# Kernel optimization log

Measured on AMD Instinct MI355X. Metric: run time of the kernel, lower is better.

The kernel has to match this reference:

```python
import jax, jax.numpy as jnp
import numpy as np


def conv2d(x, w, b):
    # x: [D, Cin, H, W], w: [Cout, Cin, kh, kw], SAME padding, stride 1
    y = jax.lax.conv_general_dilated(
        x, w, window_strides=(1, 1), padding='SAME',
        dimension_numbers=('NCHW', 'OIHW', 'NCHW'))
    return y + b[None, :, None, None]


def setup_inputs() -> dict:
    key = jax.random.key(0)
    ks = jax.random.split(key, 12)
    B, N, T, H, W = 2, 3, 16, 28, 28
    Cp, Ch, Ck, Cv, Cs = 1024, 512, 64, 512, 256
    s = 0.02
    return {
        'f16': jax.random.normal(ks[0], (B, Cp, H, W), jnp.float32),
        'mk':  jax.random.normal(ks[1], (B, Ck, T, H, W), jnp.float32),
        'mv':  jax.random.normal(ks[2], (B, N, Cv, T, H, W), jnp.float32),
        'h':   jax.random.normal(ks[3], (B, N, Cs, H, W), jnp.float32),
        # KeyProj: 1x1 conv then 3x3 conv
        'w1': jax.random.normal(ks[4], (Ch, Cp, 1, 1), jnp.float32) * s,
        'b1': jnp.zeros((Ch,), jnp.float32),
        'w2': jax.random.normal(ks[5], (Ck, Ch, 3, 3), jnp.float32) * s,
        'b2': jnp.zeros((Ck,), jnp.float32),
        # sensory-updater transform: 3x3 conv, (Cv+Cs) -> 3*Cs
        'wt': jax.random.normal(ks[6], (3 * Cs, Cv + Cs, 3, 3), jnp.float32) * s,
        'bt': jnp.zeros((3 * Cs,), jnp.float32),
    }


def reference(f16, mk, mv, h, w1, b1, w2, b2, wt, bt):
    B, Ck, T = mk.shape[0], mk.shape[1], mk.shape[2]
    N, Cv = mv.shape[1], mv.shape[2]
    Cs = h.shape[2]
    H, W = f16.shape[-2:]
    P = H * W          # query pixels
    M = T * H * W      # memory slots

    # KeyProj: query key from pixel feature
    qk = conv2d(conv2d(f16, w1, b1), w2, b2)          # [B, Ck, H, W]

    # KV-memory affinity read (softmax over memory axis)
    mk_flat = mk.reshape(B, Ck, M)
    qk_flat = qk.reshape(B, Ck, P)
    logits = jnp.einsum('bcm,bcp->bmp', mk_flat, qk_flat) / jnp.sqrt(
        jnp.asarray(Ck, qk.dtype))                     # [B, M, P]
    aff = jax.nn.softmax(logits, axis=1)               # normalize over memory
    readout = jnp.einsum('bncm,bmp->bncp', mv.reshape(B, N, Cv, M), aff)
    readout = readout.reshape(B, N, Cv, H, W)          # [B, N, Cv, H, W]

    # gated recurrent sensory update (recurrent_update)
    x = jnp.concatenate([readout, h], axis=2).reshape(B * N, Cv + Cs, H, W)
    vals = conv2d(x, wt, bt).reshape(B, N, 3 * Cs, H, W)
    forget_g = jax.nn.sigmoid(vals[:, :, :Cs])
    update_g = jax.nn.sigmoid(vals[:, :, Cs:2 * Cs])
    new_vals = jnp.tanh(vals[:, :, 2 * Cs:])
    new_h = forget_g * h * (1.0 - update_g) + update_g * new_vals
    return new_h
```

## Files before the change

kernel.cpp:

```cpp
#include <hip/hip_runtime.h>

typedef unsigned short u16;
typedef unsigned int u32;
typedef float f32x4v __attribute__((ext_vector_type(4)));
typedef __bf16 bf16x8 __attribute__((ext_vector_type(8)));

#define GAS __attribute__((address_space(1)))
#define LAS __attribute__((address_space(3)))

__device__ __forceinline__ u16 f2bf(float f) {
  u32 u = __builtin_bit_cast(u32, f);
  u32 r = (u + 0x7FFFu + ((u >> 16) & 1u)) >> 16;
  return (u16)r;
}
__device__ __forceinline__ float bf2f(u16 h) {
  return __builtin_bit_cast(float, (u32)h << 16);
}
__device__ __forceinline__ void gld_lds16(const void* g, void* l) {
  __builtin_amdgcn_global_load_lds((const GAS void*)g, (LAS void*)l, 16, 0, 0);
}
#define VMCNT(N) asm volatile("s_waitcnt vmcnt(" #N ")" ::: "memory")
#define MFMA16(a, b, c) __builtin_amdgcn_mfma_f32_16x16x32_bf16((a), (b), (c), 0, 0, 0)

template <int CONV>
__device__ __forceinline__ void gemm8p_dev(
    int lb, int Gpad, const u16* A, const u16* B, u16* Cp,
    int M, int N, int Kc, int fullK, int S,
    long strA, long strB, long strC, int Cin, int gx, int gy, int nwg, u16* smem)
{
  const int cpx = Gpad >> 3;
  const int L = (lb & 7) * cpx + (lb >> 3);
  if (L >= nwg) return;
  const int by = L % gy;
  const int rest = L / gy;
  const int bx = rest % gx;
  const int z = rest / gx;

  const int t = threadIdx.x, lane = t & 63, wave = t >> 6;
  const int zb = z / S, s = z - zb * S;
  const int m0 = bx * 256, n0 = by * 256;
  const int kbeg = s * Kc;
  const int kavail = fullK - kbeg;
  const int kc = Kc < kavail ? Kc : kavail;
  const int T = kc >> 6;

  const int srow = t >> 3;
  const int g = ((t & 7) - (srow & 7)) & 7;
  const int ldsoff = t * 8;

  const u16* Asrc[2][2];
  #pragma unroll
  for (int h = 0; h < 2; ++h)
    #pragma unroll
    for (int q = 0; q < 2; ++q) {
      int r = m0 + h * 128 + q * 64 + srow; if (r >= M) r = M - 1;
      Asrc[h][q] = A + (long)zb * strA + (long)r * fullK + kbeg + g * 8;
    }
  const u16* Bsrc[2][2];
  #pragma unroll
  for (int h = 0; h < 2; ++h)
    #pragma unroll
    for (int q = 0; q < 2; ++q) {
      if constexpr (CONV) {
        int pn = n0 + h * 128 + q * 64 + srow; if (pn >= N) pn = 0;
        const int img = pn / 784, p = pn - img * 784;
        const int py = p / 28, px = p - py * 28;
        Bsrc[h][q] = B + ((long)img * 900 + (py + 1) * 30 + (px + 1)) * Cin + g * 8;
      } else {
        int r = n0 + h * 128 + q * 64 + srow; if (r >= N) r = N - 1;
        Bsrc[h][q] = B + (long)zb * strB + (long)r * fullK + kbeg + g * 8;
      }
    }

  auto stageA = [&](int tile, int h) {
    u16* d = smem + (((tile & 1) * 2 + h) * 8192);
    const long ko = (long)tile * 64;
    gld_lds16(Asrc[h][0] + ko, d + ldsoff);
    gld_lds16(Asrc[h][1] + ko, d + 4096 + ldsoff);
  };
  auto stageB = [&](int tile, int h) {
    u16* d = smem + 32768 + (((tile & 1) * 2 + h) * 8192);
    long off;
    if constexpr (CONV) {
      const int kg = kbeg + tile * 64;
      const int tap = kg / Cin, kc2 = kg - tap * Cin;
      off = (long)((tap / 3 - 1) * 30 + (tap % 3 - 1)) * Cin + kc2;
    } else {
      off = (long)tile * 64;
    }
    gld_lds16(Bsrc[h][0] + off, d + ldsoff);
    gld_lds16(Bsrc[h][1] + off, d + 4096 + ldsoff);
  };

  const int wm = wave & 1, wn = wave >> 1;
  const int lr = lane & 15, hi = lane >> 4;
  const int slot0 = ((hi + (lr & 7)) & 7) * 8;
  const int slot1 = (((hi + 4) + (lr & 7)) & 7) * 8;
  f32x4v acc[8][4] = {};
  bf16x8 breg[4][2];

  stageB(0, 0); stageB(0, 1);
  stageA(0, 0); stageA(0, 1);
  stageB(1, 0); stageB(1, 1);
  VMCNT(4);
  __builtin_amdgcn_s_barrier();

  for (int tau = 0; tau < T; ++tau) {
    const int d = tau & 1;
    const u16* aB = smem + ((d * 2 + wm) * 8192);
    const u16* bB = smem + 32768 + ((d * 2 + (wn >> 1)) * 8192);
    const int ta = (tau + 1 < T) ? tau + 1 : T - 1;
    const int tb = (tau + 2 < T) ? tau + 2 : T - 1;
    #pragma unroll
    for (int Q = 0; Q < 4; ++Q) {
      bf16x8 aph[2][2];
      #pragma unroll
      for (int m2 = 0; m2 < 2; ++m2) {
        const int lrow = (Q * 2 + m2) * 16 + lr;
        aph[m2][0] = *(const bf16x8*)&aB[lrow * 64 + slot0];
        aph[m2][1] = *(const bf16x8*)&aB[lrow * 64 + slot1];
      }
      if (Q == 0) {
        #pragma unroll
        for (int n = 0; n < 4; ++n) {
          const int lrow = (wn & 1) * 64 + n * 16 + lr;
          breg[n][0] = *(const bf16x8*)&bB[lrow * 64 + slot0];
          breg[n][1] = *(const bf16x8*)&bB[lrow * 64 + slot1];
        }
      }
      if      (Q == 0) stageA(ta, 0);
      else if (Q == 1) stageA(ta, 1);
      else if (Q == 2) stageB(tb, 0);
      else             { stageB(tb, 1); VMCNT(4); }
      __builtin_amdgcn_sched_barrier(0);
      __builtin_amdgcn_s_barrier();
      __builtin_amdgcn_s_setprio(1);
      #pragma unroll
      for (int m2 = 0; m2 < 2; ++m2)
        #pragma unroll
        for (int n = 0; n < 4; ++n) {
          acc[Q * 2 + m2][n] = MFMA16(aph[m2][0], breg[n][0], acc[Q * 2 + m2][n]);
          acc[Q * 2 + m2][n] = MFMA16(aph[m2][1], breg[n][1], acc[Q * 2 + m2][n]);
        }
      __builtin_amdgcn_s_setprio(0);
      __builtin_amdgcn_sched_barrier(0);
      __builtin_amdgcn_s_barrier();
    }
  }
  VMCNT(0);

  u16* Co = Cp + (long)z * strC;
  #pragma unroll
  for (int m = 0; m < 8; ++m)
    #pragma unroll
    for (int r = 0; r < 4; ++r) {
      const int row = m0 + wm * 128 + m * 16 + hi * 4 + r;
      if (row >= M) continue;
      #pragma unroll
      for (int n = 0; n < 4; ++n) {
        const int col = n0 + wn * 64 + n * 16 + lr;
        if (col < N) Co[(long)row * N + col] = f2bf(acc[m][n][r]);
      }
    }
}

__device__ __forceinline__ void gemmRC_dev(
    int lb, int Gpad, const u16* A, const u16* B, u16* Cp,
    int M, int N, int Kc, int fullK, int S,
    long strA, long strB, long strC, int gx, int gy, int nwg, u16* smem)
{
  const int cpx = Gpad >> 3;
  const int L = (lb & 7) * cpx + (lb >> 3);
  if (L >= nwg) return;
  const int by = L % gy;
  const int rest = L / gy;
  const int bx = rest % gx;
  const int z = rest / gx;

  u16* sA = smem;
  u16* sB = smem + 3 * 8192;
  const int t = threadIdx.x, lane = t & 63, wave = t >> 6;
  const int zb = z / S, s = z - zb * S;
  const int m0 = bx * 256, n0 = by * 128;
  const int kbeg = s * Kc;
  const int niter = Kc >> 5;

  const int schunk = ((t & 3) ^ ((t >> 4) & 3)) * 8;
  const u16* Ap[2]; const u16* Bp;
  #pragma unroll
  for (int q = 0; q < 2; ++q) {
    int ra = m0 + q * 128 + (t >> 2); if (ra >= M) ra = M - 1;
    Ap[q] = A + (long)zb * strA + (long)ra * fullK + schunk;
  }
  {
    int rb = n0 + (t >> 2); if (rb >= N) rb = N - 1;
    Bp = B + (long)zb * strB + (long)rb * fullK + schunk;
  }
  const int ldst = t * 8;

  auto stage = [&](int buf, int kg) {
    u16* dA = sA + buf * 8192;
    gld_lds16(Ap[0] + kg, &dA[ldst]);
    gld_lds16(Ap[1] + kg, &dA[4096 + ldst]);
    gld_lds16(Bp + kg,    &sB[buf * 4096 + ldst]);
  };

  const int wrow = (wave & 3) * 64, wcol = (wave >> 2) * 64;
  const int lr = lane & 15, hi = lane >> 4;
  const int csw = (hi ^ (lr >> 2)) * 8;
  f32x4v acc[4][4] = {};

  for (int p = 0; p < 2 && p < niter; ++p) stage(p, kbeg + p * 32);
  int cur = 0, nxt = 2;
  for (int it = 0; it < niter; ++it) {
    if (it + 2 < niter) {
      stage(nxt, kbeg + (it + 2) * 32);
      VMCNT(6);
    } else {
      const int rem = niter - 1 - it;
      if (rem == 1) VMCNT(3); else VMCNT(0);
    }
    __builtin_amdgcn_s_barrier();
    __builtin_amdgcn_sched_barrier(0);
    const u16* cA = sA + cur * 8192;
    const u16* cB = sB + cur * 4096;
    bf16x8 af[4], bf[4];
    #pragma unroll
    for (int m = 0; m < 4; ++m) af[m] = *(const bf16x8*)&cA[(wrow + m*16 + lr) * 32 + csw];
    #pragma unroll
    for (int n = 0; n < 4; ++n) bf[n] = *(const bf16x8*)&cB[(wcol + n*16 + lr) * 32 + csw];
    __builtin_amdgcn_s_setprio(1);
    #pragma unroll
    for (int m = 0; m < 4; ++m)
      #pragma unroll
      for (int n = 0; n < 4; ++n)
        acc[m][n] = MFMA16(af[m], bf[n], acc[m][n]);
    __builtin_amdgcn_s_setprio(0);
    __builtin_amdgcn_sched_barrier(0);
    __builtin_amdgcn_s_barrier();
    cur = (cur + 1 == 3) ? 0 : cur + 1;
    nxt = (nxt + 1 == 3) ? 0 : nxt + 1;
  }

  u16* Co = Cp + (long)z * strC;
  const int lq = hi * 4;
  #pragma unroll
  for (int m = 0; m < 4; ++m)
    #pragma unroll
    for (int r = 0; r < 4; ++r) {
      const int row = m0 + wrow + m * 16 + lq + r;
      if (row >= M) continue;
      #pragma unroll
      for (int n = 0; n < 4; ++n) {
        const int col = n0 + wcol + n * 16 + lr;
        if (col < N) Co[(long)row * N + col] = f2bf(acc[m][n][r]);
      }
    }
}

__device__ __forceinline__ void border_slot(int slot, int& py, int& px) {
  if (slot < 30)      { py = 0;         px = slot; }
  else if (slot < 60) { py = 29;        px = slot - 30; }
  else if (slot < 88) { py = slot - 59; px = 0; }
  else                { py = slot - 87; px = 29; }
}

__device__ __forceinline__ void transp_dev(
    const float* in, u16* out, int R, int C, int ldOut,
    int bx, int by, int t, float (*tile)[33])
{
  const int c0 = bx * 32, r0 = by * 32;
  const int tx = t & 31, ty = t >> 5;
  for (int i = ty; i < 32; i += 8) {
    const int r = r0 + i, c = c0 + tx;
    tile[i][tx] = (r < R && c < C) ? in[(long)r * C + c] : 0.0f;
  }
  __syncthreads();
  for (int i = ty; i < 32; i += 8) {
    const int r = r0 + tx, c = c0 + i;
    if (c < C && r < R)
      out[(long)c * ldOut + r] = f2bf(tile[tx][i]);
  }
}

__global__ __launch_bounds__(256) void prep1(
    const float* __restrict__ f16, const float* __restrict__ mk,
    const float* __restrict__ w1, const float* __restrict__ w2,
    const float* __restrict__ wt,
    u16* __restrict__ f16T, u16* __restrict__ mkT, u16* __restrict__ w1b,
    u16* __restrict__ w2R, u16* __restrict__ wtR)
{
  __shared__ float tile[32][33];
  const int bid = blockIdx.x, t = threadIdx.x;
  if (bid < 1600) {
    const int bx = bid % 25, by = (bid / 25) % 32, bz = bid / 800;
    transp_dev(f16 + (long)bz * 1024 * 784, f16T + (long)bz * 784 * 1024,
               1024, 784, 1024, bx, by, t, tile);
    return;
  }
  if (bid < 3168) {
    const int lb = bid - 1600;
    const int bx = lb % 392, by = (lb / 392) % 2, bz = lb / 784;
    transp_dev(mk + (long)bz * 64 * 12544, mkT + (long)bz * 12544 * 64,
               64, 12544, 64, bx, by, t, tile);
    return;
  }
  if (bid < 3424) {
    const long i = (long)(bid - 3168) * 256 + t;
    const float4* p = (const float4*)w1 + i * 2;
    const float4 a = p[0], b = p[1];
    u16 o[8] = {f2bf(a.x), f2bf(a.y), f2bf(a.z), f2bf(a.w),
                f2bf(b.x), f2bf(b.y), f2bf(b.z), f2bf(b.w)};
    ((uint4*)w1b)[i] = *(uint4*)o;
    return;
  }
  if (bid < 4576) {
    const int idx = (bid - 3424) * 256 + t;
    const int c = idx % 512, tap = (idx / 512) % 9, m = idx / 4608;
    w2R[idx] = f2bf(w2[((long)m * 512 + c) * 9 + tap]);
    return;
  }
  const long idx = (long)(bid - 4576) * 256 + t;
  const int c = (int)(idx % 768), tap = (int)((idx / 768) % 9), m = (int)(idx / 6912);
  wtR[idx] = f2bf(wt[((long)m * 768 + c) * 9 + tap]);
}

__global__ __launch_bounds__(512, 4) void fused1(
    const u16* __restrict__ f16T, const u16* __restrict__ w1b,
    u16* __restrict__ parts, u16* __restrict__ out1P)
{
  extern __shared__ u16 smem[];
  const int bid = blockIdx.x, t = threadIdx.x;
  if (bid < 224) {
    gemmRC_dev(bid, 224, f16T, w1b, parts, 1568, 512, 128, 1024, 8,
               0, 0, 1568L * 512, 7, 4, 224, smem);
    return;
  }
  const int gid = (bid - 224) * 512 + t;
  if (gid < 14848) {
    const int c8 = gid & 63, rest = gid >> 6;
    const int slot = rest % 116, img = rest / 116;
    int py, px; border_slot(slot, py, px);
    *(uint4*)&out1P[((long)img * 900 + py * 30 + px) * 512 + c8 * 8] =
        make_uint4(0, 0, 0, 0);
  }
}

__global__ __launch_bounds__(256) void conv2_mv(
    const u16* __restrict__ Wt, const u16* __restrict__ imgP,
    float* __restrict__ Cp, const float* __restrict__ mv, u16* __restrict__ mvb)
{
  __shared__ u16 sA[2][128 * 32];
  __shared__ u16 sB[2][128 * 32];
  const int bid = blockIdx.x, t = threadIdx.x;
  if (bid >= 234) {
    for (long g = (long)(bid - 234) * 256 + t; g < 4816896L; g += 2048L * 256) {
      const float4* p = (const float4*)mv + g * 2;
      const float4 a = p[0], b = p[1];
      u16 o[8] = {f2bf(a.x), f2bf(a.y), f2bf(a.z), f2bf(a.w),
                  f2bf(b.x), f2bf(b.y), f2bf(b.z), f2bf(b.w)};
      ((uint4*)mvb)[g] = *(uint4*)o;
    }
    return;
  }
  const int lane = t & 63, wave = t >> 6;
  const int z = bid / 13;
  const int m0 = 0, n0 = (bid % 13) * 128;
  const int Cin = 512, Ntot = 1568, M = 64, Kc = 256;
  const int kbeg = z * Kc;

  const u16* Aptr[2]; const u16* Bptr[2]; int lofs[2];
  #pragma unroll
  for (int i = 0; i < 2; ++i) {
    const int tp = i * 256 + t;
    const int r = tp >> 2;
    const int c16 = (tp & 3) ^ ((tp >> 4) & 3);
    int ra = m0 + r; if (ra >= M) ra = M - 1;
    int pn = n0 + r; if (pn >= Ntot) pn = 0;
    const int img = pn / 784, p = pn - img * 784;
    const int py = p / 28, px = p - py * 28;
    Aptr[i] = Wt + (long)ra * (9 * Cin) + c16 * 8;
    Bptr[i] = imgP + ((long)img * 900 + (py + 1) * 30 + (px + 1)) * Cin + c16 * 8;
    lofs[i] = (i * 256 + (wave << 6)) * 8;
  }
  auto stage = [&](int buf, int kg) {
    const int tap = kg / Cin, kc = kg - tap * Cin;
    const long off = (long)((tap / 3 - 1) * 30 + (tap % 3 - 1)) * Cin + kc;
    #pragma unroll
    for (int i = 0; i < 2; ++i) {
      gld_lds16(Aptr[i] + kg, &sA[buf][lofs[i]]);
      gld_lds16(Bptr[i] + off, &sB[buf][lofs[i]]);
    }
  };

  const int wr = (wave >> 1) * 64, wc = (wave & 1) * 64;
  const int lr = lane & 15, hi = lane >> 4;
  const int csw = (hi ^ (lr >> 2)) * 8;
  f32x4v acc[4][4] = {};
  const int niter = Kc >> 5;

  stage(0, kbeg);
  for (int it = 0; it < niter; ++it) {
    const int cur = it & 1;
    if (it + 1 < niter) {
      stage(cur ^ 1, kbeg + (it + 1) * 32);
      VMCNT(4);
    } else {
      VMCNT(0);
    }
    __builtin_amdgcn_s_barrier();
    __builtin_amdgcn_sched_barrier(0);
    bf16x8 af[4], bv[4];
    #pragma unroll
    for (int i = 0; i < 4; ++i) af[i] = *(const bf16x8*)&sA[cur][(wr + i*16 + lr) * 32 + csw];
    #pragma unroll
    for (int j = 0; j < 4; ++j) bv[j] = *(const bf16x8*)&sB[cur][(wc + j*16 + lr) * 32 + csw];
    __builtin_amdgcn_s_setprio(1);
    #pragma unroll
    for (int i = 0; i < 4; ++i)
      #pragma unroll
      for (int j = 0; j < 4; ++j)
        acc[i][j] = MFMA16(af[i], bv[j], acc[i][j]);
    __builtin_amdgcn_s_setprio(0);
    __builtin_amdgcn_sched_barrier(0);
    __builtin_amdgcn_s_barrier();
  }

  float* Co = Cp + (long)z * M * Ntot;
  const int lq = hi * 4;
  #pragma unroll
  for (int i = 0; i < 4; ++i)
    #pragma unroll
    for (int r = 0; r < 4; ++r) {
      const int row = m0 + wr + i*16 + lq + r;
      if (row >= M) continue;
      #pragma unroll
      for (int j = 0; j < 4; ++j) {
        const int col = n0 + wc + j*16 + lr;
        if (col < Ntot) Co[(long)row * Ntot + col] = acc[i][j][r];
      }
    }
}

template <int BK>
__global__ __launch_bounds__(256) void gemm_glds(
    const u16* __restrict__ A, const u16* __restrict__ B, u16* __restrict__ C,
    int M, int N, int Kc, int fullK, int S,
    long strA, long strB, long strC, float scale)
{
  constexpr int CPR = BK / 8;
  constexpr int ISS = BK / 16;
  __shared__ u16 sA[2][128 * BK];
  __shared__ u16 sB[2][128 * BK];
  const int t = threadIdx.x, lane = t & 63, wave = t >> 6;
  const int z = blockIdx.z, zb = z / S;
  const int m0 = blockIdx.x * 128, n0 = blockIdx.y * 128;
  const int kbeg = (z - zb * S) * Kc;

  const u16* Aptr[ISS]; const u16* Bptr[ISS]; int lofs[ISS];
  #pragma unroll
  for (int i = 0; i < ISS; ++i) {
    const int tp = i * 256 + t;
    const int r = tp / CPR;
    int c16 = tp % CPR;
    if constexpr (BK == 32) c16 = c16 ^ ((tp >> 4) & 3);
    else                    c16 = (c16 - (r & 7)) & 7;
    int ra = m0 + r; if (ra >= M) ra = M - 1;
    int rb = n0 + r; if (rb >= N) rb = N - 1;
    Aptr[i] = A + (long)zb * strA + (long)ra * fullK + kbeg + c16 * 8;
    Bptr[i] = B + (long)zb * strB + (long)rb * fullK + kbeg + c16 * 8;
    lofs[i] = (i * 256 + (wave << 6)) * 8;
  }
  auto stage = [&](int buf, int k0) {
    #pragma unroll
    for (int i = 0; i < ISS; ++i) {
      gld_lds16(Aptr[i] + k0, &sA[buf][lofs[i]]);
      gld_lds16(Bptr[i] + k0, &sB[buf][lofs[i]]);
    }
  };

  const int wr = (wave >> 1) * 64, wc = (wave & 1) * 64;
  const int lr = lane & 15, hi = lane >> 4;
  f32x4v acc[4][4] = {};
  const int niter = Kc / BK;

  stage(0, 0);
  for (int it = 0; it < niter; ++it) {
    const int cur = it & 1;
    if (it + 1 < niter) {
      stage(cur ^ 1, (it + 1) * BK);
      if constexpr (ISS == 2) VMCNT(4); else VMCNT(8);
    } else {
      VMCNT(0);
    }
    __builtin_amdgcn_s_barrier();
    __builtin_amdgcn_sched_barrier(0);
    #pragma unroll
    for (int kk = 0; kk < BK; kk += 32) {
      bf16x8 af[4], bv[4];
      #pragma unroll
      for (int i = 0; i < 4; ++i) {
        const int row = wr + i*16 + lr;
        int lk;
        if constexpr (BK == 32) lk = kk + ((hi ^ (lr >> 2)) * 8);
        else                    lk = ((((kk >> 3) + hi) + (row & 7)) & 7) * 8;
        af[i] = *(const bf16x8*)&sA[cur][row * BK + lk];
      }
      #pragma unroll
      for (int j = 0; j < 4; ++j) {
        const int row = wc + j*16 + lr;
        int lk;
        if constexpr (BK == 32) lk = kk + ((hi ^ (lr >> 2)) * 8);
        else                    lk = ((((kk >> 3) + hi) + (row & 7)) & 7) * 8;
        bv[j] = *(const bf16x8*)&sB[cur][row * BK + lk];
      }
      __builtin_amdgcn_s_setprio(1);
      #pragma unroll
      for (int i = 0; i < 4; ++i)
        #pragma unroll
        for (int j = 0; j < 4; ++j)
          acc[i][j] = MFMA16(af[i], bv[j], acc[i][j]);
      __builtin_amdgcn_s_setprio(0);
    }
    __builtin_amdgcn_sched_barrier(0);
    __builtin_amdgcn_s_barrier();
  }

  const int lq = hi * 4;
  u16* Cw = C + (long)zb * strC;
  #pragma unroll
  for (int i = 0; i < 4; ++i)
    #pragma unroll
    for (int r = 0; r < 4; ++r) {
      const int row = m0 + wr + i*16 + lq + r;
      if (row >= M) continue;
      #pragma unroll
      for (int j = 0; j < 4; ++j) {
        const int col = n0 + wc + j*16 + lr;
        if (col < N) Cw[(long)row * N + col] = f2bf(acc[i][j][r] * scale);
      }
    }
}

__device__ __forceinline__ void addbf4(float* a, uint2 v) {
  a[0] += bf2f((u16)(v.x & 0xFFFFu));
  a[1] += bf2f((u16)(v.x >> 16));
  a[2] += bf2f((u16)(v.y & 0xFFFFu));
  a[3] += bf2f((u16)(v.y >> 16));
}

__global__ __launch_bounds__(256) void reduce_c1_bf(
    const u16* __restrict__ parts, u16* __restrict__ dst,
    const float* __restrict__ bias, int S)
{
  const long idx = (long)blockIdx.x * 256 + threadIdx.x;
  if (idx >= 1568L * 128) return;
  const int c4 = (int)(idx & 127), p = (int)(idx >> 7);
  const int c = c4 * 4;
  float sum[4] = {bias[c], bias[c+1], bias[c+2], bias[c+3]};
  for (int s = 0; s < S; ++s)
    addbf4(sum, *(const uint2*)&parts[((long)s * 1568 + p) * 512 + c]);
  const int im = p / 784, q = p - im * 784;
  const int qpad = (q / 28 + 1) * 30 + (q % 28 + 1);
  u16 o[4] = {f2bf(sum[0]), f2bf(sum[1]), f2bf(sum[2]), f2bf(sum[3])};
  *(uint2*)&dst[((long)im * 900 + qpad) * 512 + c] = *(uint2*)o;
}

__global__ __launch_bounds__(256) void reduceT_ro(
    const u16* __restrict__ parts, u16* __restrict__ dst, int S)
{
  __shared__ float tile[32][33];
  const int b = blockIdx.z, c0 = blockIdx.x * 32, p0 = blockIdx.y * 32;
  const int tx = threadIdx.x & 31, ty = threadIdx.x >> 5;
  for (int i = ty; i < 32; i += 8) {
    const int pc = min(p0 + tx, 783);
    float s = 0;
    for (int k = 0; k < S; ++k)
      s += bf2f(parts[((long)(b * S + k) * 1536 + c0 + i) * 784 + pc]);
    tile[i][tx] = s;
  }
  __syncthreads();
  for (int i = ty; i < 32; i += 8) {
    const int p = p0 + i, c = c0 + tx;
    if (p < 784) {
      const int n = c >> 9, cc = c & 511;
      const int qpad = (p / 28 + 1) * 30 + (p % 28 + 1);
      dst[((long)(b * 3 + n) * 900 + qpad) * 768 + cc] = f2bf(tile[tx][i]);
    }
  }
}

__global__ __launch_bounds__(256) void reduceT_qk(
    const float* __restrict__ parts, u16* __restrict__ dst,
    const float* __restrict__ bias, int S)
{
  __shared__ float tile[32][33];
  const int b = blockIdx.z, c0 = blockIdx.x * 32, p0 = blockIdx.y * 32;
  const int tx = threadIdx.x & 31, ty = threadIdx.x >> 5;
  for (int i = ty; i < 32; i += 8) {
    const int pc = min(p0 + tx, 783);
    const long base = (long)(c0 + i) * 1568 + b * 784 + pc;
    float s = 0;
    for (int k = 0; k < S; ++k) s += parts[(long)k * 64 * 1568 + base];
    tile[i][tx] = s;
  }
  __syncthreads();
  for (int i = ty; i < 32; i += 8) {
    const int p = p0 + i, c = c0 + tx;
    if (p < 784)
      dst[((long)b * 784 + p) * 64 + c] = f2bf(tile[tx][i] + bias[c]);
  }
}

__global__ __launch_bounds__(256) void softmax_inplace(u16* __restrict__ buf)
{
  uint4* p4 = (uint4*)(buf + (long)blockIdx.x * 12544);
  const int t = threadIdx.x;
  __shared__ float red[4];
  uint4 v[7];
  float mx = -3.0e38f;
  #pragma unroll
  for (int q = 0; q < 7; ++q) {
    const int idx = t + q * 256;
    if (idx < 1568) {
      v[q] = p4[idx];
      const u32 w[4] = {v[q].x, v[q].y, v[q].z, v[q].w};
      #pragma unroll
      for (int e = 0; e < 4; ++e) {
        mx = fmaxf(mx, bf2f((u16)(w[e] & 0xFFFFu)));
        mx = fmaxf(mx, bf2f((u16)(w[e] >> 16)));
      }
    }
  }
  #pragma unroll
  for (int o = 32; o > 0; o >>= 1) mx = fmaxf(mx, __shfl_xor(mx, o));
  if ((t & 63) == 0) red[t >> 6] = mx;
  __syncthreads();
  mx = fmaxf(fmaxf(red[0], red[1]), fmaxf(red[2], red[3]));

  float s = 0.0f;
  #pragma unroll
  for (int q = 0; q < 7; ++q) {
    const int idx = t + q * 256;
    if (idx < 1568) {
      const u32 w[4] = {v[q].x, v[q].y, v[q].z, v[q].w};
      #pragma unroll
      for (int e = 0; e < 4; ++e) {
        s += __expf(bf2f((u16)(w[e] & 0xFFFFu)) - mx);
        s += __expf(bf2f((u16)(w[e] >> 16)) - mx);
      }
    }
  }
  #pragma unroll
  for (int o = 32; o > 0; o >>= 1) s += __shfl_xor(s, o);
  __syncthreads();
  if ((t & 63) == 0) red[t >> 6] = s;
  __syncthreads();
  const float inv = 1.0f / (red[0] + red[1] + red[2] + red[3]);

  #pragma unroll
  for (int q = 0; q < 7; ++q) {
    const int idx = t + q * 256;
    if (idx < 1568) {
      u32 w[4] = {v[q].x, v[q].y, v[q].z, v[q].w};
      #pragma unroll
      for (int e = 0; e < 4; ++e) {
        const float a = __expf(bf2f((u16)(w[e] & 0xFFFFu)) - mx) * inv;
        const float b = __expf(bf2f((u16)(w[e] >> 16)) - mx) * inv;
        w[e] = (u32)f2bf(a) | ((u32)f2bf(b) << 16);
      }
      p4[idx] = make_uint4(w[0], w[1], w[2], w[3]);
    }
  }
}

__global__ __launch_bounds__(512, 2) void fused_ro(
    const u16* __restrict__ mvb, const u16* __restrict__ logaff,
    u16* __restrict__ parts, const float* __restrict__ hin,
    u16* __restrict__ concatP, int Kc, int S)
{
  extern __shared__ u16 smem[];
  const int bid = blockIdx.x, t = threadIdx.x;
  if (bid < 240) {
    gemm8p_dev<0>(bid, 240, mvb, logaff, parts, 1536, 784, Kc, 12544, S,
                  1536L * 12544, 784L * 12544, 1536L * 784, 0, 6, 4, 240, smem);
    return;
  }
  int lb = bid - 240;
  if (lb < 1200) {
    float (*tile)[33] = (float(*)[33])smem;
    const int bx = lb % 8, by = (lb / 8) % 25, zimg = lb / 200;
    const int c0 = bx * 32, p0 = by * 32;
    const int tx = t & 31, ty = t >> 5;
    for (int i = ty; i < 32; i += 16) {
      const int pc = min(p0 + tx, 783);
      tile[i][tx] = hin[((long)zimg * 256 + c0 + i) * 784 + pc];
    }
    __syncthreads();
    for (int i = ty; i < 32; i += 16) {
      const int p = p0 + i, c = c0 + tx;
      if (p < 784) {
        const int qpad = (p / 28 + 1) * 30 + (p % 28 + 1);
        concatP[((long)zimg * 900 + qpad) * 768 + 512 + c] = f2bf(tile[tx][i]);
      }
    }
    return;
  }
  lb -= 1200;
  const int gid = lb * 512 + t;
  if (gid < 66816) {
    const int c8 = gid % 96, rest = gid / 96;
    const int slot = rest % 116, img = rest / 116;
    int py, px; border_slot(slot, py, px);
    *(uint4*)&concatP[((long)img * 900 + py * 30 + px) * 768 + c8 * 8] =
        make_uint4(0, 0, 0, 0);
  }
}

__global__ __launch_bounds__(512, 2) void gemm8p_tr(
    const u16* __restrict__ A, const u16* __restrict__ B, u16* __restrict__ Cp,
    int M, int N, int Kc, int fullK, int S,
    long strC, int Cin, int gx, int gy, int nwg)
{
  extern __shared__ u16 smem[];
  gemm8p_dev<1>(blockIdx.x, (int)gridDim.x, A, B, Cp, M, N, Kc, fullK, S,
                0, 0, strC, Cin, gx, gy, nwg, smem);
}

__global__ __launch_bounds__(256) void treduce_gate(
    const u16* __restrict__ parts, const float* __restrict__ bt,
    const float* __restrict__ h, float* __restrict__ out, int S)
{
  const long i = (long)blockIdx.x * 256 + threadIdx.x;
  if (i >= 6L * 256 * 196) return;
  const int p4 = (int)(i % 196);
  const int rest = (int)(i / 196);
  const int cs = rest % 256, im = rest / 256;
  const long slice = 768L * 4704;
  const long pbase = (long)im * 784 + p4 * 4;
  float F[4] = {}, U[4] = {}, NV[4] = {};
  for (int s = 0; s < S; ++s) {
    const u16* P = parts + (long)s * slice;
    addbf4(F,  *(const uint2*)&P[(long)cs         * 4704 + pbase]);
    addbf4(U,  *(const uint2*)&P[(long)(256 + cs) * 4704 + pbase]);
    addbf4(NV, *(const uint2*)&P[(long)(512 + cs) * 4704 + pbase]);
  }
  const float bF = bt[cs], bU = bt[256 + cs], bN = bt[512 + cs];
  const f32x4v hv = ((const f32x4v*)h)[((long)(im * 256 + cs) * 784 >> 2) + p4];
  f32x4v o;
  #pragma unroll
  for (int q = 0; q < 4; ++q) {
    const float f = F[q] + bF, u = U[q] + bU, nv = NV[q] + bN;
    const float sf = 1.0f / (1.0f + __expf(-f));
    const float su = 1.0f / (1.0f + __expf(-u));
    const float e2 = __expf(2.0f * nv);
    const float tv = (e2 - 1.0f) / (e2 + 1.0f);
    o[q] = sf * hv[q] * (1.0f - su) + su * tv;
  }
  ((f32x4v*)out)[((long)(im * 256 + cs) * 784 >> 2) + p4] = o;
}

__global__ __launch_bounds__(256) void fill_sentinel(float* p, long n) {
  const long i = (long)blockIdx.x * 256 + threadIdx.x;
  if (i < n) p[i] = 12345.0f;
}

extern "C" void kernel_launch(void* const* d_in, const int* in_sizes, int n_in,
                              void* d_out, int out_size, void* d_ws, size_t ws_size,
                              hipStream_t stream) {
  const float* f16 = (const float*)d_in[0];
  const float* mk  = (const float*)d_in[1];
  const float* mv  = (const float*)d_in[2];
  const float* hin = (const float*)d_in[3];
  const float* w1  = (const float*)d_in[4];
  const float* b1  = (const float*)d_in[5];
  const float* w2  = (const float*)d_in[6];
  const float* b2  = (const float*)d_in[7];
  const float* wt  = (const float*)d_in[8];
  const float* bt  = (const float*)d_in[9];
  float* out = (float*)d_out;

  (void)hipFuncSetAttribute((const void*)fused1,
                            hipFuncAttributeMaxDynamicSharedMemorySize, 73728);
  (void)hipFuncSetAttribute((const void*)fused_ro,
                            hipFuncAttributeMaxDynamicSharedMemorySize, 131072);
  (void)hipFuncSetAttribute((const void*)gemm8p_tr,
                            hipFuncAttributeMaxDynamicSharedMemorySize, 131072);
  constexpr unsigned DSMR = 73728, DSM8 = 131072;

  const size_t B_f16T   = 2UL*784*1024*2;
  const size_t B_w1b    = 512UL*1024*2;
  const size_t B_w2R    = 64UL*4608*2;
  const size_t B_out1P  = 2UL*900*512*2;
  const size_t B_qkT    = 2UL*784*64*2;
  const size_t B_concat = 6UL*900*768*2;
  const size_t B_wtR    = 768UL*6912*2;
  const size_t B_mkT    = 2UL*12544*64*2;
  const size_t B_logaff = 2UL*784*12544*2;
  const size_t B_mvb    = 38535168UL*2;
  auto al = [](size_t x) { return (x + 255) & ~(size_t)255; };

  const size_t phase1 = al(B_f16T) + al(B_w1b) + al(B_w2R) + al(B_out1P) + al(B_qkT);
  const size_t regionA = phase1 > al(B_concat) ? phase1 : al(B_concat);

  const int S_ro = 5, S_tr = 4, S_c1 = 8;
  const int Kc_ro = 2560, Kc_tr = 1728;
  auto poolBytes = [&]() -> size_t {
    size_t p2 = 18UL*64*1568*4;
    size_t p1 = (size_t)S_c1*1568*512*2;
    size_t pr = (size_t)(2*S_ro)*1536*784*2;
    size_t pt = (size_t)S_tr*768*4704*2;
    size_t m = p2; if (p1 > m) m = p1; if (pr > m) m = pr; if (pt > m) m = pt;
    return m;
  };
  const size_t fixed = regionA + al(B_wtR) + al(B_mkT) + al(B_logaff) + al(B_mvb);
  if (fixed + poolBytes() > ws_size) {
    fill_sentinel<<<4704, 256, 0, stream>>>(out, (long)out_size);
    return;
  }

  char* base = (char*)d_ws;
  size_t off = 0;
  auto alloc = [&](size_t bytes) -> char* { char* p = base + off; off += al(bytes); return p; };
  char* rA = alloc(regionA);
  u16* f16T   = (u16*)rA;
  u16* w1b    = (u16*)(rA + al(B_f16T));
  u16* w2R    = (u16*)(rA + al(B_f16T) + al(B_w1b));
  u16* out1P  = (u16*)(rA + al(B_f16T) + al(B_w1b) + al(B_w2R));
  u16* qkT    = (u16*)(rA + al(B_f16T) + al(B_w1b) + al(B_w2R) + al(B_out1P));
  u16* concatP = (u16*)rA;
  u16*   wtR     = (u16*)alloc(B_wtR);
  u16*   mkT     = (u16*)alloc(B_mkT);
  u16*   logaff  = (u16*)alloc(B_logaff);
  u16*   mvb     = (u16*)alloc(B_mvb);
  char*  partsRaw = alloc(poolBytes());
  float* partsF  = (float*)partsRaw;
  u16*   partsH  = (u16*)partsRaw;

  prep1<<<25312, 256, 0, stream>>>(f16, mk, w1, w2, wt, f16T, mkT, w1b, w2R, wtR);

  fused1<<<253, 512, DSMR, stream>>>(f16T, w1b, partsH, out1P);

  reduce_c1_bf<<<784, 256, 0, stream>>>(partsH, out1P, b1, S_c1);

  conv2_mv<<<2282, 256, 0, stream>>>(w2R, out1P, partsF, mv, mvb);

  reduceT_qk<<<dim3(2, 25, 2), 256, 0, stream>>>(partsF, qkT, b2, 18);

  gemm_glds<64><<<dim3(7, 98, 2), 256, 0, stream>>>(
      qkT, mkT, logaff, 784, 12544, 64, 64, 1,
      784L*64, 12544L*64, 784L*12544, 0.125f);

  softmax_inplace<<<1568, 256, 0, stream>>>(logaff);

  fused_ro<<<1571, 512, DSM8, stream>>>(mvb, logaff, partsH, hin, concatP,
                                        Kc_ro, S_ro);

  reduceT_ro<<<dim3(48, 25, 2), 256, 0, stream>>>(partsH, concatP, S_ro);

  gemm8p_tr<<<232, 512, DSM8, stream>>>(wtR, concatP, partsH,
                                        768, 4704, Kc_tr, 6912, S_tr,
                                        768L*4704, 768, 3, 19, 228);

  treduce_gate<<<1176, 256, 0, stream>>>(partsH, bt, hin, out, S_tr);
}
```

Baseline: 300.0 us.

## Move mv bf16 cast into prep1 and stage weight reorders through LDS

The fp32-to-bf16 cast of mv moves out of the conv2 kernel and into the prep1 kernel, so conv2 now runs only its 234 GEMM blocks. The w2 and wt tap reorders now read each output-channel row into shared memory with coalesced loads and write it back in the permuted order, instead of doing strided scalar gathers. Together these cut the prep1 grid size, though enlarging shared memory to 27 KB per block may lower occupancy for the transpose blocks.

```diff
diff --git a/kernel.cpp b/kernel.cpp
--- a/kernel.cpp
+++ b/kernel.cpp
@@ -286,23 +286,23 @@
 __global__ __launch_bounds__(256) void prep1(
     const float* __restrict__ f16, const float* __restrict__ mk,
     const float* __restrict__ w1, const float* __restrict__ w2,
-    const float* __restrict__ wt,
+    const float* __restrict__ wt, const float* __restrict__ mv,
     u16* __restrict__ f16T, u16* __restrict__ mkT, u16* __restrict__ w1b,
-    u16* __restrict__ w2R, u16* __restrict__ wtR)
-{
-  __shared__ float tile[32][33];
+    u16* __restrict__ w2R, u16* __restrict__ wtR, u16* __restrict__ mvb)
+{
+  __shared__ float scratch[6912];
   const int bid = blockIdx.x, t = threadIdx.x;
   if (bid < 1600) {
     const int bx = bid % 25, by = (bid / 25) % 32, bz = bid / 800;
     transp_dev(f16 + (long)bz * 1024 * 784, f16T + (long)bz * 784 * 1024,
-               1024, 784, 1024, bx, by, t, tile);
+               1024, 784, 1024, bx, by, t, (float(*)[33])scratch);
     return;
   }
   if (bid < 3168) {
     const int lb = bid - 1600;
     const int bx = lb % 392, by = (lb / 392) % 2, bz = lb / 784;
     transp_dev(mk + (long)bz * 64 * 12544, mkT + (long)bz * 12544 * 64,
-               64, 12544, 64, bx, by, t, tile);
+               64, 12544, 64, bx, by, t, (float(*)[33])scratch);
     return;
   }
   if (bid < 3424) {
@@ -314,15 +314,42 @@
     ((uint4*)w1b)[i] = *(uint4*)o;
     return;
   }
-  if (bid < 4576) {
-    const int idx = (bid - 3424) * 256 + t;
-    const int c = idx % 512, tap = (idx / 512) % 9, m = idx / 4608;
-    w2R[idx] = f2bf(w2[((long)m * 512 + c) * 9 + tap]);
+  if (bid < 3488) {
+    const int m = bid - 3424;
+    const float* src = w2 + (long)m * 4608;
+    for (int j = t; j < 4608; j += 256) scratch[j] = src[j];
+    __syncthreads();
+    u16* dst = w2R + (long)m * 4608;
+    #pragma unroll
+    for (int tap = 0; tap < 9; ++tap)
+      for (int c = t; c < 512; c += 256)
+        dst[tap * 512 + c] = f2bf(scratch[c * 9 + tap]);
     return;
   }
-  const long idx = (long)(bid - 4576) * 256 + t;
-  const int c = (int)(idx % 768), tap = (int)((idx / 768) % 9), m = (int)(idx / 6912);
-  wtR[idx] = f2bf(wt[((long)m * 768 + c) * 9 + tap]);
+  if (bid < 4256) {
+    const int m = bid - 3488;
+    const float* src = wt + (long)m * 6912;
+    for (int j = t; j < 6912; j += 256) scratch[j] = src[j];
+    __syncthreads();
+    u16* dst = wtR + (long)m * 6912;
+    #pragma unroll
+    for (int tap = 0; tap < 9; ++tap)
+      for (int c = t; c < 768; c += 256)
+        dst[tap * 768 + c] = f2bf(scratch[c * 9 + tap]);
+    return;
+  }
+  {
+    const long g0 = (long)(bid - 4256) * 512 + t;
+    #pragma unroll
+    for (int k = 0; k < 2; ++k) {
+      const long g = g0 + k * 256;
+      const float4* p = (const float4*)mv + g * 2;
+      const float4 a = p[0], b = p[1];
+      u16 o[8] = {f2bf(a.x), f2bf(a.y), f2bf(a.z), f2bf(a.w),
+                  f2bf(b.x), f2bf(b.y), f2bf(b.z), f2bf(b.w)};
+      ((uint4*)mvb)[g] = *(uint4*)o;
+    }
+  }
 }
 
 __global__ __launch_bounds__(512, 4) void fused1(
@@ -346,23 +373,13 @@
   }
 }
 
-__global__ __launch_bounds__(256) void conv2_mv(
+__global__ __launch_bounds__(256) void conv2_k(
     const u16* __restrict__ Wt, const u16* __restrict__ imgP,
-    float* __restrict__ Cp, const float* __restrict__ mv, u16* __restrict__ mvb)
+    float* __restrict__ Cp)
 {
   __shared__ u16 sA[2][128 * 32];
   __shared__ u16 sB[2][128 * 32];
   const int bid = blockIdx.x, t = threadIdx.x;
-  if (bid >= 234) {
-    for (long g = (long)(bid - 234) * 256 + t; g < 4816896L; g += 2048L * 256) {
-      const float4* p = (const float4*)mv + g * 2;
-      const float4 a = p[0], b = p[1];
-      u16 o[8] = {f2bf(a.x), f2bf(a.y), f2bf(a.z), f2bf(a.w),
-                  f2bf(b.x), f2bf(b.y), f2bf(b.z), f2bf(b.w)};
-      ((uint4*)mvb)[g] = *(uint4*)o;
-    }
-    return;
-  }
   const int lane = t & 63, wave = t >> 6;
   const int z = bid / 13;
   const int m0 = 0, n0 = (bid % 13) * 128;
@@ -837,13 +854,14 @@
   float* partsF  = (float*)partsRaw;
   u16*   partsH  = (u16*)partsRaw;
 
-  prep1<<<25312, 256, 0, stream>>>(f16, mk, w1, w2, wt, f16T, mkT, w1b, w2R, wtR);
+  prep1<<<13664, 256, 0, stream>>>(f16, mk, w1, w2, wt, mv,
+                                   f16T, mkT, w1b, w2R, wtR, mvb);
 
   fused1<<<253, 512, DSMR, stream>>>(f16T, w1b, partsH, out1P);
 
   reduce_c1_bf<<<784, 256, 0, stream>>>(partsH, out1P, b1, S_c1);
 
-  conv2_mv<<<2282, 256, 0, stream>>>(w2R, out1P, partsF, mv, mvb);
+  conv2_k<<<234, 256, 0, stream>>>(w2R, out1P, partsF);
 
   reduceT_qk<<<dim3(2, 25, 2), 256, 0, stream>>>(partsF, qkT, b2, 18);
 
```

After: 289.4 us. 1.04x faster.
